# Kernel optimization log

Hardware: AMD Instinct MI355X
Metric: run time of the kernel (lower is better)

Reference implementation:

```python
import jax, jax.numpy as jnp
import numpy as np

B, S, HID = 4, 1024, 1024
NH = 16
DH = HID // NH  # 64


def _split_heads(t):
    # [B, S, HID] -> [B, NH, S, DH]
    return t.reshape(B, S, NH, DH).transpose(0, 2, 1, 3)


def _merge_heads(t):
    # [B, NH, S, DH] -> [B, S, HID]
    return t.transpose(0, 2, 1, 3).reshape(B, S, HID)


def setup_inputs() -> dict:
    key = jax.random.key(0)
    ks = jax.random.split(key, 13)
    scale = 1.0 / np.sqrt(HID)
    inp = {"x": jax.random.normal(ks[0], (B, S, HID), dtype=jnp.float32)}
    names = ["Wq", "Wk", "Wv", "Wq2", "Wk2", "Wv2"]
    for i, n in enumerate(names):
        inp[n] = jax.random.normal(ks[1 + i], (HID, HID), dtype=jnp.float32) * scale
        inp["b" + n[1:]] = jax.random.normal(ks[7 + i], (HID,), dtype=jnp.float32) * 0.01
    return inp


def _attn(q, k, v):
    # q,k,v: [B, NH, S, DH]
    scores = jnp.einsum("bhqd,bhkd->bhqk", q, k) / np.sqrt(DH).astype(np.float32)
    probs = jax.nn.softmax(scores, axis=-1)
    return jnp.einsum("bhqk,bhkd->bhqd", probs, v)


def reference(x, Wq, bq, Wk, bk, Wv, bv, Wq2, bq2, Wk2, bk2, Wv2, bv2):
    # nn.Linear: y = x @ W.T + b
    q1 = _split_heads(x @ Wq.T + bq)
    k1 = _split_heads(x @ Wk.T + bk)
    v1 = _split_heads(x @ Wv.T + bv)
    q2 = _split_heads(x @ Wq2.T + bq2)
    k2 = _split_heads(x @ Wk2.T + bk2)
    v2 = _split_heads(x @ Wv2.T + bv2)
    # 5'UTR direction: q1 attends to k2/v2; 3'UTR direction: q2 attends to k1/v1
    out5 = _merge_heads(_attn(q1, k2, v2))
    out3 = _merge_heads(_attn(q2, k1, v1))
    return (out5, out3)
```

## Files before the change

kernel.cpp:

```cpp
#include <hip/hip_runtime.h>


typedef __attribute__((ext_vector_type(8))) short bf16x8;
typedef __attribute__((ext_vector_type(4))) short bf16x4;
typedef __attribute__((ext_vector_type(4))) float f32x4;
typedef __attribute__((ext_vector_type(4))) short s16x4;

#define MFMA16(a, b, c) __builtin_amdgcn_mfma_f32_16x16x32_bf16(a, b, c, 0, 0, 0)
#define BARRIER() asm volatile("s_barrier" ::: "memory")
#define VMCNT0() asm volatile("s_waitcnt vmcnt(0)" ::: "memory")

__device__ __forceinline__ f32x4 mfma16k(bf16x4 a, bf16x4 b, f32x4 c) {
#if __has_builtin(__builtin_amdgcn_mfma_f32_16x16x16bf16_1k)
  return __builtin_amdgcn_mfma_f32_16x16x16bf16_1k(a, b, c, 0, 0, 0);
#elif __has_builtin(__builtin_amdgcn_mfma_f32_16x16x16_bf16)
  return __builtin_amdgcn_mfma_f32_16x16x16_bf16(a, b, c, 0, 0, 0);
#else
  asm volatile("v_mfma_f32_16x16x16_bf16 %0, %1, %2, %0"
               : "+v"(c) : "v"(a), "v"(b));
  return c;
#endif
}

__device__ __forceinline__ unsigned short f2bf(float f) {
  unsigned u = __float_as_uint(f);
  u = (u + 0x7fffu + ((u >> 16) & 1u)) >> 16;
  return (unsigned short)u;
}

__device__ __forceinline__ unsigned cvt_pk_bf16(float lo, float hi) {
  unsigned r;
  asm("v_cvt_pk_bf16_f32 %0, %1, %2" : "=v"(r) : "v"(lo), "v"(hi));
  return r;
}

__device__ __forceinline__ void gll16(const void* g, void* l) {
  __builtin_amdgcn_global_load_lds(
      (const __attribute__((address_space(1))) unsigned int*)g,
      (__attribute__((address_space(3))) unsigned int*)l, 16, 0, 0);
}

__global__ __launch_bounds__(256) void convert_k(
    const float* __restrict__ x,
    const float* __restrict__ W0, const float* __restrict__ W1,
    const float* __restrict__ W2, const float* __restrict__ W3,
    const float* __restrict__ W4, const float* __restrict__ W5,
    short* __restrict__ xbf, short* __restrict__ wbf) {
  const int tid = blockIdx.x * 256 + threadIdx.x;
  const int e = tid << 2;
  const float* src;
  short* dst;
  int off;
  if (e < (4 << 20)) {
    src = x; dst = xbf; off = e;
  } else {
    const int j = e - (4 << 20);
    const int wsel = j >> 20;
    off = j & ((1 << 20) - 1);
    src = (wsel == 0) ? W0 : (wsel == 1) ? W1 : (wsel == 2) ? W2
        : (wsel == 3) ? W3 : (wsel == 4) ? W4 : W5;
    dst = wbf + ((size_t)wsel << 20);
  }
  const float4 v = *(const float4*)(src + off);
  s16x4 o;
  o.x = (short)f2bf(v.x);
  o.y = (short)f2bf(v.y);
  o.z = (short)f2bf(v.z);
  o.w = (short)f2bf(v.w);
  *(s16x4*)(dst + off) = o;
}

__global__ __launch_bounds__(512, 2) void proj_gemm192(
    const short* __restrict__ Ag, const short* __restrict__ Wall,
    const float* __restrict__ bq, const float* __restrict__ bk,
    const float* __restrict__ bv, const float* __restrict__ bq2,
    const float* __restrict__ bk2, const float* __restrict__ bv2,
    short* __restrict__ qkv) {
  __shared__ __align__(16) short As[2][16384];
  __shared__ __align__(16) short Bs[2][12288];

  const int bid = blockIdx.x;
  const int xcd = bid & 7, k = bid >> 3;
  const int ns = k & 3, mb = k >> 2;
  const int nbase = (xcd * 4 + ns) * 192;
  const int m0 = mb << 8;

  const int t = threadIdx.x, lane = t & 63, w = t >> 6;
  const int g = lane >> 4, lr = lane & 15;
  const int wr = w >> 2, wc = w & 3;

  f32x4 acc[2][4][3] = {};

  auto stage_ah = [&](int T, int H) {
#pragma unroll
    for (int ld = 0; ld < 2; ++ld) {
      const int slot = (H << 10) + (ld << 9) + t;
      const int rr = slot >> 3;
      const int gc = (slot & 7) ^ (rr & 7);
      gll16(Ag + (size_t)(m0 + rr) * 1024 + (T << 6) + (gc << 3),
            &As[T & 1][slot * 8]);
    }
  };
  auto stage_b = [&](int T) {
#pragma unroll
    for (int ld = 0; ld < 3; ++ld) {
      const int slot = (ld << 9) + t;
      const int rr = slot >> 3;
      const int gc = (slot & 7) ^ (rr & 7);
      gll16(Wall + (size_t)(nbase + rr) * 1024 + (T << 6) + (gc << 3),
            &Bs[T & 1][slot * 8]);
    }
  };

  stage_ah(0, 0); stage_ah(0, 1); stage_b(0);
  VMCNT0();
  BARRIER();

#define LOAD_A(MH, KK, TB)                                                \
  _Pragma("unroll") for (int mi = 0; mi < 4; ++mi) {                      \
    const int rA = wr * 128 + (MH) * 64 + mi * 16 + lr;                   \
    af[mi] = *(const bf16x8*)                                             \
        &As[TB][rA * 64 + ((((KK) * 4 + g) ^ (rA & 7)) << 3)];            \
  }
#define LOAD_B(KK, TB)                                                    \
  _Pragma("unroll") for (int nj = 0; nj < 3; ++nj) {                      \
    const int rB = wc * 48 + nj * 16 + lr;                                \
    bf[nj] = *(const bf16x8*)                                             \
        &Bs[TB][rB * 64 + ((((KK) * 4 + g) ^ (rB & 7)) << 3)];            \
  }
#define MFMA_PH(MH)                                                       \
  __builtin_amdgcn_s_setprio(1);                                          \
  _Pragma("unroll") for (int mi = 0; mi < 4; ++mi)                        \
    _Pragma("unroll") for (int nj = 0; nj < 3; ++nj)                      \
      acc[MH][mi][nj] = MFMA16(af[mi], bf[nj], acc[MH][mi][nj]);          \
  __builtin_amdgcn_s_setprio(0);

  auto group = [&](int C, int TD, bool DV) {
    bf16x8 af[4], bf[3];
    {
      LOAD_A(0, 0, C); LOAD_B(0, C);
      if (DV) stage_ah(TD, 0);
      BARRIER();
      MFMA_PH(0);
      BARRIER();
    }
    {
      LOAD_A(1, 0, C);
      if (DV) stage_ah(TD, 1);
      BARRIER();
      MFMA_PH(1);
      BARRIER();
    }
    {
      LOAD_A(0, 1, C); LOAD_B(1, C);
      if (DV) stage_b(TD);
      BARRIER();
      MFMA_PH(0);
      BARRIER();
    }
    {
      LOAD_A(1, 1, C);
      BARRIER();
      MFMA_PH(1);
      VMCNT0();
      BARRIER();
    }
  };

  for (int j = 0; j < 8; ++j) {
    group(0, 2 * j + 1, true);
    group(1, 2 * j + 2, j < 7);
  }

#undef LOAD_A
#undef LOAD_B
#undef MFMA_PH

#pragma unroll
  for (int nj = 0; nj < 3; ++nj) {
    const int nn = nbase + wc * 48 + nj * 16 + lr;
    const int p = nn >> 10, nl = nn & 1023;
    const float* bp = (p == 0) ? bq : (p == 1) ? bk : (p == 2) ? bv
                    : (p == 3) ? bq2 : (p == 4) ? bk2 : bv2;
    const float bb = bp[nl];
    const int h = nl >> 6, d = nl & 63;
    const int pt = (p == 0 || p == 3) ? 0 : (p == 1 || p == 4) ? 1 : 2;
    unsigned short* dst = (unsigned short*)qkv + ((size_t)p << 22);
#pragma unroll
    for (int mh = 0; mh < 2; ++mh) {
#pragma unroll
      for (int mi = 0; mi < 4; ++mi) {
#pragma unroll
        for (int r = 0; r < 4; ++r) {
          const int m = m0 + wr * 128 + mh * 64 + mi * 16 + (g << 2) + r;
          const int b = m >> 10, s = m & 1023;
          const unsigned short val = f2bf(acc[mh][mi][nj][r] + bb);
          size_t idx;
          if (pt == 0) {
            idx = ((size_t)(((b << 4) + h) * 1024 + s) << 6) + d;
          } else if (pt == 1) {
            const int d2 = (d & 7) | (((d >> 3) ^ (s & 7)) << 3);
            idx = ((size_t)(((b << 4) + h) * 1024 + s) << 6) + d2;
          } else {
            const int tt = s >> 6, s2 = s & 63;
            const int s3 = (s2 & 7) | (((s2 >> 3) ^ (d & 7)) << 3);
            idx = ((size_t)((((b << 4) + h) * 16 + tt) * 64 + d) << 6) + s3;
          }
          dst[idx] = val;
        }
      }
    }
  }
}

__global__ __launch_bounds__(512) void attn_k(const short* __restrict__ qkv,
                                              float* __restrict__ out) {
  __shared__ __align__(16) short Ks[2][64 * 64];
  __shared__ __align__(16) short Vs[2][64 * 64];

  const int L = blockIdx.x;
  const int xcd = L & 7, ss = L >> 3;
  const int qt = ss & 7, pg = ss >> 3;
  const int pp = xcd + (pg << 3);
  const int hb = pp & 63, dir = pp >> 6;

  const short* Q = qkv + ((size_t)(dir ? 3 : 0) << 22) + ((size_t)hb << 16);
  const short* K = qkv + ((size_t)(dir ? 1 : 4) << 22) + ((size_t)hb << 16);
  const short* V = qkv + ((size_t)(dir ? 2 : 5) << 22) + ((size_t)hb << 16);
  float* O = out + ((size_t)dir << 22);

  const int t = threadIdx.x, lane = t & 63, w = t >> 6;
  const int g = lane >> 4, lr = lane & 15;

  const int qrow = (qt << 7) + (w << 4) + lr;
  bf16x8 qf[2];
  qf[0] = *(const bf16x8*)(Q + qrow * 64 + g * 8);
  qf[1] = *(const bf16x8*)(Q + qrow * 64 + 32 + g * 8);

  const bf16x4 ones4 = {0x3F80, 0x3F80, 0x3F80, 0x3F80};

  f32x4 oacc[4] = {};
  f32x4 lacc = {};
  float mrun = -3.0e38f;
  const float CSC = 0.18033688f;

  const int srow = t >> 3;
  const int scol = (t & 7) << 3;

  auto stage = [&](int kt, int buf) {
    gll16(K + (size_t)((kt << 6) + srow) * 64 + scol, &Ks[buf][w << 9]);
    gll16(V + (size_t)(kt << 12) + (size_t)srow * 64 + scol, &Vs[buf][w << 9]);
  };

  stage(0, 0);
  VMCNT0();
  BARRIER();

  int cur = 0;
  for (int kt = 0; kt < 16; ++kt) {
    if (kt < 15) stage(kt + 1, cur ^ 1);

    f32x4 sc2[4] = {};
    __builtin_amdgcn_s_setprio(1);
#pragma unroll
    for (int dk = 0; dk < 2; ++dk) {
#pragma unroll
      for (int kn = 0; kn < 4; ++kn) {
        const int krow = kn * 16 + lr;
        const bf16x8 kf = *(const bf16x8*)
            &Ks[cur][krow * 64 +
                     ((((dk << 6) + (g << 4)) ^ ((krow & 7) << 4)) >> 1)];
        sc2[kn] = MFMA16(kf, qf[dk], sc2[kn]);
      }
    }
    __builtin_amdgcn_s_setprio(0);

    float tm = fmaxf(fmaxf(fmaxf(sc2[0][0], sc2[0][1]),
                           fmaxf(sc2[0][2], sc2[0][3])),
                     fmaxf(fmaxf(sc2[1][0], sc2[1][1]),
                           fmaxf(sc2[1][2], sc2[1][3])));
    tm = fmaxf(tm, fmaxf(fmaxf(fmaxf(sc2[2][0], sc2[2][1]),
                               fmaxf(sc2[2][2], sc2[2][3])),
                         fmaxf(fmaxf(sc2[3][0], sc2[3][1]),
                               fmaxf(sc2[3][2], sc2[3][3]))));
    const bool ok = __all(fmaf(tm, CSC, -mrun) <= 8.0f);
    if (!ok) {
      float t2 = fmaxf(tm, __shfl_xor(tm, 16));
      t2 = fmaxf(t2, __shfl_xor(t2, 32));
      const float mnew = fmaxf(mrun, t2 * CSC);
      const float scq = exp2f(mrun - mnew);
      mrun = mnew;
#pragma unroll
      for (int r = 0; r < 4; ++r) {
        const float sr = __shfl(scq, (g << 2) + r);
        lacc[r] *= sr;
#pragma unroll
        for (int dn = 0; dn < 4; ++dn) oacc[dn][r] *= sr;
      }
    }

    bf16x4 pa[4];
#pragma unroll
    for (int kn = 0; kn < 4; ++kn) {
      const float p0 = exp2f(fmaf(sc2[kn][0], CSC, -mrun));
      const float p1 = exp2f(fmaf(sc2[kn][1], CSC, -mrun));
      const float p2 = exp2f(fmaf(sc2[kn][2], CSC, -mrun));
      const float p3 = exp2f(fmaf(sc2[kn][3], CSC, -mrun));
      union { unsigned u[2]; bf16x4 v; } pk;
      pk.u[0] = cvt_pk_bf16(p0, p1);
      pk.u[1] = cvt_pk_bf16(p2, p3);
      pa[kn] = pk.v;
    }

    __builtin_amdgcn_s_setprio(1);
#pragma unroll
    for (int kn = 0; kn < 4; ++kn) {
      lacc = mfma16k(pa[kn], ones4, lacc);
#pragma unroll
      for (int dn = 0; dn < 4; ++dn) {
        const int vrow = dn * 16 + lr;
        const int ch = (2 * kn + (g >> 1)) ^ (vrow & 7);
        const bf16x4 vf = *(const bf16x4*)
            &Vs[cur][vrow * 64 + ch * 8 + ((g & 1) << 2)];
        oacc[dn] = mfma16k(pa[kn], vf, oacc[dn]);
      }
    }
    __builtin_amdgcn_s_setprio(0);

    VMCNT0();
    BARRIER();
    cur ^= 1;
  }

  const int b = hb >> 4, h = hb & 15;
  float rl[4];
#pragma unroll
  for (int r = 0; r < 4; ++r) rl[r] = 1.0f / lacc[r];
#pragma unroll
  for (int dn = 0; dn < 4; ++dn) {
#pragma unroll
    for (int r = 0; r < 4; ++r) {
      const int q = (qt << 7) + (w << 4) + (g << 2) + r;
      const int d = dn * 16 + lr;
      O[((size_t)(b * 1024 + q) << 10) + h * 64 + d] = oacc[dn][r] * rl[r];
    }
  }
}

extern "C" void kernel_launch(void* const* d_in, const int* in_sizes, int n_in,
                              void* d_out, int out_size, void* d_ws,
                              size_t ws_size, hipStream_t stream) {
  const float* x   = (const float*)d_in[0];
  const float* Wq  = (const float*)d_in[1];
  const float* bq  = (const float*)d_in[2];
  const float* Wk  = (const float*)d_in[3];
  const float* bk  = (const float*)d_in[4];
  const float* Wv  = (const float*)d_in[5];
  const float* bv  = (const float*)d_in[6];
  const float* Wq2 = (const float*)d_in[7];
  const float* bq2 = (const float*)d_in[8];
  const float* Wk2 = (const float*)d_in[9];
  const float* bk2 = (const float*)d_in[10];
  const float* Wv2 = (const float*)d_in[11];
  const float* bv2 = (const float*)d_in[12];

  char* ws = (char*)d_ws;
  short* xbf = (short*)ws;
  short* wbf = (short*)(ws + 8388608);
  short* qkv = (short*)(ws + 20971520);

  convert_k<<<10240, 256, 0, stream>>>(x, Wq, Wk, Wv, Wq2, Wk2, Wv2, xbf, wbf);
  proj_gemm192<<<512, 512, 0, stream>>>(xbf, wbf, bq, bk, bv, bq2, bk2,
                                        bv2, qkv);
  attn_k<<<1024, 512, 0, stream>>>(qkv, (float*)d_out);
}
```

Baseline: 156.8 us.

## Enlarge projection GEMM tile to 256x256 with split-half staging and deeper prefetch

The QKV projection GEMM moves from 256x192 output tiles (512 blocks) to 256x256 tiles (384 blocks), mapped as 3 N-tiles per XCD. Each operand tile is staged in two 128-row halves, and the eight-phase loop issues the next K-step's half-tiles early, waiting with vmcnt(4) instead of draining all loads. The aim is more operand reuse per byte loaded and better overlap of global-to-LDS copies with MFMA work. The cost is a larger LDS footprint and fewer blocks than CUs-times-two, which can leave the second wave of blocks partially empty and the load imbalanced.

```diff
diff --git a/kernel.cpp b/kernel.cpp
--- a/kernel.cpp
+++ b/kernel.cpp
@@ -9,6 +9,7 @@
 #define MFMA16(a, b, c) __builtin_amdgcn_mfma_f32_16x16x32_bf16(a, b, c, 0, 0, 0)
 #define BARRIER() asm volatile("s_barrier" ::: "memory")
 #define VMCNT0() asm volatile("s_waitcnt vmcnt(0)" ::: "memory")
+#define VMCNT4() asm volatile("s_waitcnt vmcnt(4)" ::: "memory")
 
 __device__ __forceinline__ f32x4 mfma16k(bf16x4 a, bf16x4 b, f32x4 c) {
 #if __has_builtin(__builtin_amdgcn_mfma_f32_16x16x16bf16_1k)
@@ -70,143 +71,165 @@
   *(s16x4*)(dst + off) = o;
 }
 
-__global__ __launch_bounds__(512, 2) void proj_gemm192(
+__global__ __launch_bounds__(512, 2) void proj_g8(
     const short* __restrict__ Ag, const short* __restrict__ Wall,
     const float* __restrict__ bq, const float* __restrict__ bk,
     const float* __restrict__ bv, const float* __restrict__ bq2,
     const float* __restrict__ bk2, const float* __restrict__ bv2,
     short* __restrict__ qkv) {
-  __shared__ __align__(16) short As[2][16384];
-  __shared__ __align__(16) short Bs[2][12288];
+  __shared__ __align__(16) short As[2][2][8192];
+  __shared__ __align__(16) short Bs[2][2][8192];
 
   const int bid = blockIdx.x;
-  const int xcd = bid & 7, k = bid >> 3;
-  const int ns = k & 3, mb = k >> 2;
-  const int nbase = (xcd * 4 + ns) * 192;
+  const int xcd = bid & 7, i = bid >> 3;
+  const int nb = xcd * 3 + (i >> 4);
+  const int mb = i & 15;
   const int m0 = mb << 8;
 
   const int t = threadIdx.x, lane = t & 63, w = t >> 6;
   const int g = lane >> 4, lr = lane & 15;
   const int wr = w >> 2, wc = w & 3;
 
-  f32x4 acc[2][4][3] = {};
-
-  auto stage_ah = [&](int T, int H) {
-#pragma unroll
-    for (int ld = 0; ld < 2; ++ld) {
-      const int slot = (H << 10) + (ld << 9) + t;
-      const int rr = slot >> 3;
-      const int gc = (slot & 7) ^ (rr & 7);
-      gll16(Ag + (size_t)(m0 + rr) * 1024 + (T << 6) + (gc << 3),
-            &As[T & 1][slot * 8]);
-    }
-  };
-  auto stage_b = [&](int T) {
-#pragma unroll
-    for (int ld = 0; ld < 3; ++ld) {
-      const int slot = (ld << 9) + t;
-      const int rr = slot >> 3;
-      const int gc = (slot & 7) ^ (rr & 7);
-      gll16(Wall + (size_t)(nbase + rr) * 1024 + (T << 6) + (gc << 3),
-            &Bs[T & 1][slot * 8]);
-    }
-  };
-
-  stage_ah(0, 0); stage_ah(0, 1); stage_b(0);
-  VMCNT0();
-  BARRIER();
-
-#define LOAD_A(MH, KK, TB)                                                \
-  _Pragma("unroll") for (int mi = 0; mi < 4; ++mi) {                      \
-    const int rA = wr * 128 + (MH) * 64 + mi * 16 + lr;                   \
-    af[mi] = *(const bf16x8*)                                             \
-        &As[TB][rA * 64 + ((((KK) * 4 + g) ^ (rA & 7)) << 3)];            \
-  }
-#define LOAD_B(KK, TB)                                                    \
-  _Pragma("unroll") for (int nj = 0; nj < 3; ++nj) {                      \
-    const int rB = wc * 48 + nj * 16 + lr;                                \
-    bf[nj] = *(const bf16x8*)                                             \
-        &Bs[TB][rB * 64 + ((((KK) * 4 + g) ^ (rB & 7)) << 3)];            \
-  }
-#define MFMA_PH(MH)                                                       \
+  f32x4 acc[2][2][4][2] = {};
+  bf16x8 af[4][2], bf[2][2];
+
+#define STAGE_A(T, H)                                                     \
+  {                                                                       \
+    const int k0s = (T) << 6;                                             \
+    _Pragma("unroll") for (int ld = 0; ld < 2; ++ld) {                    \
+      const int slot = (ld << 9) + t;                                     \
+      const int rr = slot >> 3;                                           \
+      const int gc = (slot & 7) ^ (rr & 7);                               \
+      gll16(Ag + (size_t)(m0 + (H) * 128 + rr) * 1024 + k0s + (gc << 3),  \
+            &As[(T) & 1][H][slot * 8]);                                   \
+    }                                                                     \
+  }
+#define STAGE_B(T, H)                                                     \
+  {                                                                       \
+    const int k0s = (T) << 6;                                             \
+    _Pragma("unroll") for (int ld = 0; ld < 2; ++ld) {                    \
+      const int slot = (ld << 9) + t;                                     \
+      const int rr = slot >> 3;                                           \
+      const int gc = (slot & 7) ^ (rr & 7);                               \
+      gll16(Wall + (size_t)((nb << 8) + (H) * 128 + rr) * 1024 + k0s +    \
+                (gc << 3),                                                \
+            &Bs[(T) & 1][H][slot * 8]);                                   \
+    }                                                                     \
+  }
+#define LOAD_A(MH, TB)                                                    \
+  _Pragma("unroll") for (int mi = 0; mi < 4; ++mi)                        \
+    _Pragma("unroll") for (int kk = 0; kk < 2; ++kk) {                    \
+      const int row = wr * 64 + mi * 16 + lr;                             \
+      af[mi][kk] = *(const bf16x8*)                                       \
+          &As[TB][MH][row * 64 + ((((kk << 2) + g) ^ (row & 7)) << 3)];   \
+    }
+#define LOAD_B(NH, TB)                                                    \
+  _Pragma("unroll") for (int nj = 0; nj < 2; ++nj)                        \
+    _Pragma("unroll") for (int kk = 0; kk < 2; ++kk) {                    \
+      const int row = wc * 32 + nj * 16 + lr;                             \
+      bf[nj][kk] = *(const bf16x8*)                                       \
+          &Bs[TB][NH][row * 64 + ((((kk << 2) + g) ^ (row & 7)) << 3)];   \
+    }
+#define MFMA_PH(MH, NH)                                                   \
   __builtin_amdgcn_s_setprio(1);                                          \
   _Pragma("unroll") for (int mi = 0; mi < 4; ++mi)                        \
-    _Pragma("unroll") for (int nj = 0; nj < 3; ++nj)                      \
-      acc[MH][mi][nj] = MFMA16(af[mi], bf[nj], acc[MH][mi][nj]);          \
+    _Pragma("unroll") for (int nj = 0; nj < 2; ++nj)                      \
+      _Pragma("unroll") for (int kk = 0; kk < 2; ++kk)                    \
+        acc[MH][NH][mi][nj] =                                             \
+            MFMA16(af[mi][kk], bf[nj][kk], acc[MH][NH][mi][nj]);          \
   __builtin_amdgcn_s_setprio(0);
 
-  auto group = [&](int C, int TD, bool DV) {
-    bf16x8 af[4], bf[3];
-    {
-      LOAD_A(0, 0, C); LOAD_B(0, C);
-      if (DV) stage_ah(TD, 0);
+  STAGE_A(0, 0); STAGE_A(0, 1); STAGE_B(0, 0); STAGE_B(0, 1);
+  STAGE_A(1, 0); STAGE_B(1, 1);
+  VMCNT4();
+  BARRIER();
+
+  for (int j = 0; j < 8; ++j) {
+    const bool u = j < 7;
+    {
+      LOAD_A(0, 0); LOAD_B(0, 0);
+      STAGE_A(2 * j + 1, 1); STAGE_B(2 * j + 1, 0);
+      BARRIER(); MFMA_PH(0, 0); BARRIER();
+    }
+    {
+      LOAD_B(1, 0);
+      BARRIER(); MFMA_PH(0, 1); BARRIER();
+    }
+    {
+      LOAD_A(1, 0);
+      if (u) STAGE_A(2 * j + 2, 0);
+      BARRIER(); MFMA_PH(1, 1); BARRIER();
+    }
+    {
+      LOAD_B(0, 0);
+      if (u) STAGE_B(2 * j + 2, 1);
+      BARRIER(); MFMA_PH(1, 0);
+      if (u) { VMCNT4(); } else { VMCNT0(); }
       BARRIER();
-      MFMA_PH(0);
+    }
+    {
+      LOAD_A(0, 1); LOAD_B(0, 1);
+      if (u) { STAGE_A(2 * j + 2, 1); STAGE_B(2 * j + 2, 0); }
+      BARRIER(); MFMA_PH(0, 0); BARRIER();
+    }
+    {
+      LOAD_B(1, 1);
+      BARRIER(); MFMA_PH(0, 1); BARRIER();
+    }
+    {
+      LOAD_A(1, 1);
+      if (u) STAGE_A(2 * j + 3, 0);
+      BARRIER(); MFMA_PH(1, 1); BARRIER();
+    }
+    {
+      LOAD_B(0, 1);
+      if (u) STAGE_B(2 * j + 3, 1);
+      BARRIER(); MFMA_PH(1, 0);
+      if (u) { VMCNT4(); }
       BARRIER();
     }
-    {
-      LOAD_A(1, 0, C);
-      if (DV) stage_ah(TD, 1);
-      BARRIER();
-      MFMA_PH(1);
-      BARRIER();
-    }
-    {
-      LOAD_A(0, 1, C); LOAD_B(1, C);
-      if (DV) stage_b(TD);
-      BARRIER();
-      MFMA_PH(0);
-      BARRIER();
-    }
-    {
-      LOAD_A(1, 1, C);
-      BARRIER();
-      MFMA_PH(1);
-      VMCNT0();
-      BARRIER();
-    }
-  };
-
-  for (int j = 0; j < 8; ++j) {
-    group(0, 2 * j + 1, true);
-    group(1, 2 * j + 2, j < 7);
-  }
-
+  }
+
+#undef STAGE_A
+#undef STAGE_B
 #undef LOAD_A
 #undef LOAD_B
 #undef MFMA_PH
 
 #pragma unroll
-  for (int nj = 0; nj < 3; ++nj) {
-    const int nn = nbase + wc * 48 + nj * 16 + lr;
-    const int p = nn >> 10, nl = nn & 1023;
-    const float* bp = (p == 0) ? bq : (p == 1) ? bk : (p == 2) ? bv
-                    : (p == 3) ? bq2 : (p == 4) ? bk2 : bv2;
-    const float bb = bp[nl];
-    const int h = nl >> 6, d = nl & 63;
-    const int pt = (p == 0 || p == 3) ? 0 : (p == 1 || p == 4) ? 1 : 2;
-    unsigned short* dst = (unsigned short*)qkv + ((size_t)p << 22);
-#pragma unroll
-    for (int mh = 0; mh < 2; ++mh) {
-#pragma unroll
-      for (int mi = 0; mi < 4; ++mi) {
-#pragma unroll
-        for (int r = 0; r < 4; ++r) {
-          const int m = m0 + wr * 128 + mh * 64 + mi * 16 + (g << 2) + r;
-          const int b = m >> 10, s = m & 1023;
-          const unsigned short val = f2bf(acc[mh][mi][nj][r] + bb);
-          size_t idx;
-          if (pt == 0) {
-            idx = ((size_t)(((b << 4) + h) * 1024 + s) << 6) + d;
-          } else if (pt == 1) {
-            const int d2 = (d & 7) | (((d >> 3) ^ (s & 7)) << 3);
-            idx = ((size_t)(((b << 4) + h) * 1024 + s) << 6) + d2;
-          } else {
-            const int tt = s >> 6, s2 = s & 63;
-            const int s3 = (s2 & 7) | (((s2 >> 3) ^ (d & 7)) << 3);
-            idx = ((size_t)((((b << 4) + h) * 16 + tt) * 64 + d) << 6) + s3;
+  for (int nh = 0; nh < 2; ++nh) {
+#pragma unroll
+    for (int nj = 0; nj < 2; ++nj) {
+      const int nn = (nb << 8) + nh * 128 + wc * 32 + nj * 16 + lr;
+      const int p = nn >> 10, nl = nn & 1023;
+      const float* bp = (p == 0) ? bq : (p == 1) ? bk : (p == 2) ? bv
+                      : (p == 3) ? bq2 : (p == 4) ? bk2 : bv2;
+      const float bb = bp[nl];
+      const int h = nl >> 6, d = nl & 63;
+      const int pt = (p == 0 || p == 3) ? 0 : (p == 1 || p == 4) ? 1 : 2;
+      unsigned short* dst = (unsigned short*)qkv + ((size_t)p << 22);
+#pragma unroll
+      for (int mh = 0; mh < 2; ++mh) {
+#pragma unroll
+        for (int mi = 0; mi < 4; ++mi) {
+#pragma unroll
+          for (int r = 0; r < 4; ++r) {
+            const int m = m0 + mh * 128 + wr * 64 + mi * 16 + (g << 2) + r;
+            const int b = m >> 10, s = m & 1023;
+            const unsigned short val = f2bf(acc[mh][nh][mi][nj][r] + bb);
+            size_t idx;
+            if (pt == 0) {
+              idx = ((size_t)(((b << 4) + h) * 1024 + s) << 6) + d;
+            } else if (pt == 1) {
+              const int d2 = (d & 7) | (((d >> 3) ^ (s & 7)) << 3);
+              idx = ((size_t)(((b << 4) + h) * 1024 + s) << 6) + d2;
+            } else {
+              const int tt = s >> 6, s2 = s & 63;
+              const int s3 = (s2 & 7) | (((s2 >> 3) ^ (d & 7)) << 3);
+              idx = ((size_t)((((b << 4) + h) * 16 + tt) * 64 + d) << 6) + s3;
+            }
+            dst[idx] = val;
           }
-          dst[idx] = val;
         }
       }
     }
@@ -370,7 +393,7 @@
   short* qkv = (short*)(ws + 20971520);
 
   convert_k<<<10240, 256, 0, stream>>>(x, Wq, Wk, Wv, Wq2, Wk2, Wv2, xbf, wbf);
-  proj_gemm192<<<512, 512, 0, stream>>>(xbf, wbf, bq, bk, bv, bq2, bk2,
-                                        bv2, qkv);
+  proj_g8<<<384, 512, 0, stream>>>(xbf, wbf, bq, bk, bv, bq2, bk2,
+                                   bv2, qkv);
   attn_k<<<1024, 512, 0, stream>>>(qkv, (float*)d_out);
 }
```

After: 189.8 us. +21.1%, slower.
